# Kernel optimization log

Measured on AMD Instinct MI355X. Metric: run time of the kernel, lower is better.

Reference implementation:

```python
import jax, jax.numpy as jnp
import numpy as np

N_USERS = 100_000
N_ENTITIES = 400_000
N_NODES = N_USERS + N_ENTITIES  # 500k
DIM = 64
N_EDGES = 2_000_000
BATCH = 4096
N_LAYERS = 3
CF_WEIGHT = 1.0
L2_REG = 1e-4


def setup_inputs() -> dict:
    key = jax.random.key(0)
    k_emb, k_e, k_u, k_p, k_n = jax.random.split(key, 5)
    # xavier_uniform on (N, D): bound = sqrt(6/(N+D))
    bound = float(np.sqrt(6.0 / (N_NODES + DIM)))
    emb = jax.random.uniform(k_emb, (N_NODES, DIM), jnp.float32, -bound, bound)
    edge_index = jax.random.randint(k_e, (2, N_EDGES), 0, N_NODES, dtype=jnp.int32)
    user_idx = jax.random.randint(k_u, (BATCH,), 0, N_USERS, dtype=jnp.int32)
    pos_item = jax.random.randint(k_p, (BATCH,), 0, N_NODES, dtype=jnp.int32)
    neg_item = jax.random.randint(k_n, (BATCH,), 0, N_NODES, dtype=jnp.int32)
    return {"emb": emb, "edge_index": edge_index, "user_idx": user_idx,
            "pos_item": pos_item, "neg_item": neg_item}


def _lightgcn(emb, edge_index, n_layers):
    # LGConv(normalize=True): x' = D^{-1/2} A D^{-1/2} x, no self loops.
    n = emb.shape[0]
    src, dst = edge_index[0], edge_index[1]
    deg = jax.ops.segment_sum(jnp.ones_like(dst, dtype=emb.dtype), dst,
                              num_segments=n)
    dinv = jnp.where(deg > 0, jax.lax.rsqrt(jnp.maximum(deg, 1e-12)), 0.0)
    norm = dinv[src] * dinv[dst]  # [E]
    x = emb
    acc = emb  # layer-0 term of the mean over stacked layers
    for _ in range(n_layers):
        msgs = x[src] * norm[:, None]  # [E, D] gather + scale
        x = jax.ops.segment_sum(msgs, dst, num_segments=n)  # scatter-add
        acc = acc + x
    return acc / (n_layers + 1)  # mean over (layers+1) stacked embeddings


def reference(emb, edge_index, user_idx, pos_item, neg_item):
    all_layer = _lightgcn(emb, edge_index, N_LAYERS)
    u = all_layer[user_idx]
    p = all_layer[pos_item]
    n_ = all_layer[neg_item]
    pos_score = jnp.sum(u * p, axis=-1)
    neg_score = jnp.sum(u * n_, axis=-1)
    # BPRLoss: -mean(logsigmoid(pos - neg)) == mean(softplus(neg - pos))
    cf_loss = jnp.mean(jax.nn.softplus(neg_score - pos_score))
    u_ego = emb[user_idx]
    p_ego = emb[pos_item]
    n_ego = emb[neg_item]
    reg_loss = 0.5 * (jnp.sum(u_ego ** 2) + jnp.sum(p_ego ** 2)
                      + jnp.sum(n_ego ** 2)) / float(BATCH)
    return CF_WEIGHT * cf_loss + L2_REG * reg_loss
```

## Files before the change

kernel.cpp:

```cpp
#include <hip/hip_runtime.h>
#include <cstdint>
#include <cstddef>

#define N_USERS   100000
#define N_NODES   500000
#define DIM       64
#define N_EDGES   2000000
#define BATCH     4096
#define SCAN_B    1024
#define NBLK      ((N_NODES + SCAN_B - 1) / SCAN_B)
#define X1C_CAP   350000
#define LA_CAP    150000

__global__ void k_deg(const int* __restrict__ dst, int* __restrict__ deg) {
    int t = blockIdx.x * blockDim.x + threadIdx.x;
    if (t < N_EDGES / 4) {
        int4 d = ((const int4*)dst)[t];
        atomicAdd(&deg[d.x], 1); atomicAdd(&deg[d.y], 1);
        atomicAdd(&deg[d.z], 1); atomicAdd(&deg[d.w], 1);
    }
}

__global__ void k_scan1(const int* __restrict__ v, int* __restrict__ bsum) {
    __shared__ int s[SCAN_B];
    int i = blockIdx.x * SCAN_B + threadIdx.x;
    s[threadIdx.x] = (i < N_NODES) ? v[i] : 0;
    __syncthreads();
    for (int off = SCAN_B / 2; off; off >>= 1) {
        if (threadIdx.x < off) s[threadIdx.x] += s[threadIdx.x + off];
        __syncthreads();
    }
    if (threadIdx.x == 0) bsum[blockIdx.x] = s[0];
}

__global__ void k_scan2(const int* __restrict__ bsum, int* __restrict__ boff,
                        int* __restrict__ tail, int tail_val) {
    __shared__ int s[512];
    int v = (threadIdx.x < NBLK) ? bsum[threadIdx.x] : 0;
    s[threadIdx.x] = v;
    __syncthreads();
    for (int off = 1; off < 512; off <<= 1) {
        int t = (threadIdx.x >= off) ? s[threadIdx.x - off] : 0;
        __syncthreads();
        s[threadIdx.x] += t;
        __syncthreads();
    }
    if (threadIdx.x < NBLK) boff[threadIdx.x] = s[threadIdx.x] - v;
    if (threadIdx.x == 0 && tail) tail[0] = tail_val;
}

__global__ void k_scan3(const int* __restrict__ deg, const int* __restrict__ boff,
                        int* __restrict__ rowstart, int* __restrict__ cursor,
                        float* __restrict__ dinv) {
    __shared__ int s[SCAN_B];
    int i = blockIdx.x * SCAN_B + threadIdx.x;
    int v = (i < N_NODES) ? deg[i] : 0;
    s[threadIdx.x] = v;
    __syncthreads();
    for (int off = 1; off < SCAN_B; off <<= 1) {
        int t = (threadIdx.x >= off) ? s[threadIdx.x - off] : 0;
        __syncthreads();
        s[threadIdx.x] += t;
        __syncthreads();
    }
    if (i < N_NODES) {
        int ex = s[threadIdx.x] - v + boff[blockIdx.x];
        rowstart[i] = ex;
        cursor[i] = ex;
        dinv[i] = (v > 0) ? rsqrtf((float)v) : 0.0f;
    }
}

__global__ void k_scan1f(const unsigned char* __restrict__ fA,
                         const unsigned char* __restrict__ fB,
                         int* __restrict__ bsumP) {
    __shared__ int s[SCAN_B];
    int i = blockIdx.x * SCAN_B + threadIdx.x;
    int v = 0;
    if (i < N_NODES) v = (int)fA[i] | ((int)fB[i] << 16);
    s[threadIdx.x] = v;
    __syncthreads();
    for (int off = SCAN_B / 2; off; off >>= 1) {
        if (threadIdx.x < off) s[threadIdx.x] += s[threadIdx.x + off];
        __syncthreads();
    }
    if (threadIdx.x == 0) bsumP[blockIdx.x] = s[0];
}

__global__ void k_scan2f(const int* __restrict__ bsumP, int* __restrict__ boffA,
                         int* __restrict__ boffB, int* __restrict__ counts) {
    __shared__ int sA[512];
    __shared__ int sB[512];
    int p = (threadIdx.x < NBLK) ? bsumP[threadIdx.x] : 0;
    int vA = p & 0xFFFF, vB = p >> 16;
    sA[threadIdx.x] = vA; sB[threadIdx.x] = vB;
    __syncthreads();
    for (int off = 1; off < 512; off <<= 1) {
        int tA = (threadIdx.x >= off) ? sA[threadIdx.x - off] : 0;
        int tB = (threadIdx.x >= off) ? sB[threadIdx.x - off] : 0;
        __syncthreads();
        sA[threadIdx.x] += tA; sB[threadIdx.x] += tB;
        __syncthreads();
    }
    if (threadIdx.x < NBLK) {
        boffA[threadIdx.x] = sA[threadIdx.x] - vA;
        boffB[threadIdx.x] = sB[threadIdx.x] - vB;
    }
    if (threadIdx.x == 511) { counts[0] = sA[511]; counts[1] = sB[511]; }
}

__global__ void k_scan3f(const unsigned char* __restrict__ fA,
                         const unsigned char* __restrict__ fB,
                         const int* __restrict__ boffA, const int* __restrict__ boffB,
                         int* __restrict__ mapB, int* __restrict__ listA,
                         int* __restrict__ listB) {
    __shared__ int s[SCAN_B];
    int i = blockIdx.x * SCAN_B + threadIdx.x;
    int a = 0, b = 0;
    if (i < N_NODES) { a = (int)fA[i]; b = (int)fB[i]; }
    int v = a | (b << 16);
    s[threadIdx.x] = v;
    __syncthreads();
    for (int off = 1; off < SCAN_B; off <<= 1) {
        int t = (threadIdx.x >= off) ? s[threadIdx.x - off] : 0;
        __syncthreads();
        s[threadIdx.x] += t;
        __syncthreads();
    }
    if (i < N_NODES) {
        int inc = s[threadIdx.x];
        int exA = (inc & 0xFFFF) - a + boffA[blockIdx.x];
        int exB = (inc >> 16) - b + boffB[blockIdx.x];
        if (a) listA[exA] = i;
        mapB[i] = b ? exB : -1;
        if (b) listB[exB] = i;
    }
}

__global__ void k_scatter(const int* __restrict__ src, const int* __restrict__ dst,
                          const unsigned char* __restrict__ fB,
                          int* __restrict__ cursor, int* __restrict__ csr_src) {
    int t = blockIdx.x * blockDim.x + threadIdx.x;
    if (t < N_EDGES / 4) {
        int4 s = ((const int4*)src)[t];
        int4 d = ((const int4*)dst)[t];
        if (fB[d.x]) csr_src[atomicAdd(&cursor[d.x], 1)] = s.x;
        if (fB[d.y]) csr_src[atomicAdd(&cursor[d.y], 1)] = s.y;
        if (fB[d.z]) csr_src[atomicAdd(&cursor[d.z], 1)] = s.z;
        if (fB[d.w]) csr_src[atomicAdd(&cursor[d.w], 1)] = s.w;
    }
}

__global__ void k_mark(const int* __restrict__ u, const int* __restrict__ p,
                       const int* __restrict__ n, unsigned char* __restrict__ f3,
                       unsigned char* __restrict__ fA, unsigned char* __restrict__ fB) {
    int i = blockIdx.x * blockDim.x + threadIdx.x;
    if (i >= 3 * BATCH) return;
    int idx;
    if (i < BATCH)          idx = u[i];
    else if (i < 2 * BATCH) idx = p[i - BATCH];
    else                    idx = n[i - 2 * BATCH];
    f3[idx] = 1; fA[idx] = 1; fB[idx] = 1;
}

__global__ void k_expand_edges(const int* __restrict__ src, const int* __restrict__ dst,
                               const unsigned char* __restrict__ fin,
                               unsigned char* __restrict__ fout) {
    int t = blockIdx.x * blockDim.x + threadIdx.x;
    if (t < N_EDGES / 4) {
        int4 s = ((const int4*)src)[t];
        int4 d = ((const int4*)dst)[t];
        if (fin[d.x] && !fout[s.x]) fout[s.x] = 1;
        if (fin[d.y] && !fout[s.y]) fout[s.y] = 1;
        if (fin[d.z] && !fout[s.z]) fout[s.z] = 1;
        if (fin[d.w] && !fout[s.w]) fout[s.w] = 1;
    }
}

__global__ void k_prop1(const float* __restrict__ emb, const int* __restrict__ listB,
                        const int* __restrict__ counts,
                        const float* __restrict__ dinv, const int* __restrict__ rowstart,
                        const int* __restrict__ csr_src, float* __restrict__ x1c) {
    int lane = threadIdx.x & 63;
    int wv = (blockIdx.x * blockDim.x + threadIdx.x) >> 6;
    if (wv >= counts[1]) return;
    int node = listB[wv];
    int sub = lane >> 4, q = lane & 15;
    int b = rowstart[node], e = rowstart[node + 1];
    float4 acc = {0.f, 0.f, 0.f, 0.f};
    for (int i = b + sub; i < e; i += 4) {
        int s = csr_src[i];
        float dv = dinv[s];
        float4 v = ((const float4*)(emb + (size_t)s * DIM))[q];
        acc.x += v.x * dv; acc.y += v.y * dv; acc.z += v.z * dv; acc.w += v.w * dv;
    }
    for (int off = 16; off <= 32; off <<= 1) {
        acc.x += __shfl_xor(acc.x, off, 64);
        acc.y += __shfl_xor(acc.y, off, 64);
        acc.z += __shfl_xor(acc.z, off, 64);
        acc.w += __shfl_xor(acc.w, off, 64);
    }
    if (sub == 0) {
        float dw = dinv[node];
        float4 o = {acc.x * dw, acc.y * dw, acc.z * dw, acc.w * dw};
        ((float4*)x1c)[(size_t)wv * 16 + q] = o;
    }
}

__global__ void k_prop2(const float* __restrict__ x1c, const int* __restrict__ mapB,
                        const int* __restrict__ listA, const int* __restrict__ counts,
                        const float* __restrict__ dinv, const int* __restrict__ rowstart,
                        const int* __restrict__ csr_src, float* __restrict__ x2) {
    int lane = threadIdx.x & 63;
    int wv = (blockIdx.x * blockDim.x + threadIdx.x) >> 6;
    if (wv >= counts[0]) return;
    int node = listA[wv];
    int sub = lane >> 4, q = lane & 15;
    int b = rowstart[node], e = rowstart[node + 1];
    float4 acc = {0.f, 0.f, 0.f, 0.f};
    for (int i = b + sub; i < e; i += 4) {
        int s = csr_src[i];
        float dv = dinv[s];
        float4 v = ((const float4*)(x1c + (size_t)mapB[s] * DIM))[q];
        acc.x += v.x * dv; acc.y += v.y * dv; acc.z += v.z * dv; acc.w += v.w * dv;
    }
    for (int off = 16; off <= 32; off <<= 1) {
        acc.x += __shfl_xor(acc.x, off, 64);
        acc.y += __shfl_xor(acc.y, off, 64);
        acc.z += __shfl_xor(acc.z, off, 64);
        acc.w += __shfl_xor(acc.w, off, 64);
    }
    if (sub == 0) {
        float dw = dinv[node];
        float4 o = {acc.x * dw, acc.y * dw, acc.z * dw, acc.w * dw};
        ((float4*)(x2 + (size_t)node * DIM))[q] = o;
    }
}

__global__ void k_prop3(const float* __restrict__ x2,
                        const int* __restrict__ u, const int* __restrict__ p,
                        const int* __restrict__ n,
                        const float* __restrict__ dinv, const int* __restrict__ rowstart,
                        const int* __restrict__ csr_src, float* __restrict__ x3c) {
    int lane = threadIdx.x & 63;
    int wv = (blockIdx.x * blockDim.x + threadIdx.x) >> 6;
    if (wv >= 3 * BATCH) return;
    int t;
    if (wv < BATCH)          t = u[wv];
    else if (wv < 2 * BATCH) t = p[wv - BATCH];
    else                     t = n[wv - 2 * BATCH];
    int sub = lane >> 4, q = lane & 15;
    int b = rowstart[t], e = rowstart[t + 1];
    float4 acc = {0.f, 0.f, 0.f, 0.f};
    for (int i = b + sub; i < e; i += 4) {
        int s = csr_src[i];
        float dv = dinv[s];
        float4 v = ((const float4*)(x2 + (size_t)s * DIM))[q];
        acc.x += v.x * dv; acc.y += v.y * dv; acc.z += v.z * dv; acc.w += v.w * dv;
    }
    for (int off = 16; off <= 32; off <<= 1) {
        acc.x += __shfl_xor(acc.x, off, 64);
        acc.y += __shfl_xor(acc.y, off, 64);
        acc.z += __shfl_xor(acc.z, off, 64);
        acc.w += __shfl_xor(acc.w, off, 64);
    }
    if (sub == 0) {
        float dw = dinv[t];
        float4 o = {acc.x * dw, acc.y * dw, acc.z * dw, acc.w * dw};
        ((float4*)x3c)[(size_t)wv * 16 + q] = o;
    }
}

__global__ void k_loss(const float* __restrict__ emb, const float* __restrict__ x1c,
                       const float* __restrict__ x2, const float* __restrict__ x3c,
                       const int* __restrict__ mapB,
                       const int* __restrict__ u, const int* __restrict__ p,
                       const int* __restrict__ n, float* __restrict__ out) {
    int lane = threadIdx.x & 63;
    int w = (blockIdx.x * blockDim.x + threadIdx.x) >> 6;
    if (w >= BATCH) return;
    int ui = u[w], pi = p[w], ni = n[w];
    float ue = emb[(size_t)ui * DIM + lane];
    float pe = emb[(size_t)pi * DIM + lane];
    float ne = emb[(size_t)ni * DIM + lane];
    float uall = 0.25f * (ue + x1c[(size_t)mapB[ui] * DIM + lane]
                             + x2[(size_t)ui * DIM + lane]
                             + x3c[(size_t)w * DIM + lane]);
    float pall = 0.25f * (pe + x1c[(size_t)mapB[pi] * DIM + lane]
                             + x2[(size_t)pi * DIM + lane]
                             + x3c[(size_t)(BATCH + w) * DIM + lane]);
    float nall = 0.25f * (ne + x1c[(size_t)mapB[ni] * DIM + lane]
                             + x2[(size_t)ni * DIM + lane]
                             + x3c[(size_t)(2 * BATCH + w) * DIM + lane]);
    float pos = uall * pall;
    float neg = uall * nall;
    float sq  = ue * ue + pe * pe + ne * ne;
    for (int off = 32; off; off >>= 1) {
        pos += __shfl_xor(pos, off, 64);
        neg += __shfl_xor(neg, off, 64);
        sq  += __shfl_xor(sq,  off, 64);
    }
    if (lane == 0) {
        float z = neg - pos;
        float sp = fmaxf(z, 0.0f) + log1pf(expf(-fabsf(z)));
        float contrib = sp * (1.0f / BATCH) + 1e-4f * 0.5f * sq * (1.0f / BATCH);
        atomicAdd(out, contrib);
    }
}

extern "C" void kernel_launch(void* const* d_in, const int* in_sizes, int n_in,
                              void* d_out, int out_size, void* d_ws, size_t ws_size,
                              hipStream_t stream) {
    const float* emb  = (const float*)d_in[0];
    const int*   edge = (const int*)d_in[1];
    const int*   src  = edge;
    const int*   dst  = edge + N_EDGES;
    const int*   uidx = (const int*)d_in[2];
    const int*   pidx = (const int*)d_in[3];
    const int*   nidx = (const int*)d_in[4];
    float* out = (float*)d_out;

    char* w = (char*)d_ws;
    float* x2       = (float*)w;                 w += (size_t)N_NODES * DIM * 4;
    float* x1c      = (float*)w;                 w += (size_t)X1C_CAP * DIM * 4;
    float* x3c      = (float*)w;                 w += (size_t)3 * BATCH * DIM * 4;
    float* dinv     = (float*)w;                 w += (size_t)N_NODES * 4;
    int*   deg      = (int*)w;                   w += (size_t)N_NODES * 4;
    int*   rowstart = (int*)w;                   w += (size_t)(N_NODES + 4) * 4;
    int*   cursor   = (int*)w;                   w += (size_t)N_NODES * 4;
    int*   csr_src  = (int*)w;                   w += (size_t)N_EDGES * 4;
    int*   mapB     = (int*)w;                   w += (size_t)N_NODES * 4;
    int*   listB    = (int*)w;                   w += (size_t)X1C_CAP * 4;
    int*   listA    = (int*)w;                   w += (size_t)LA_CAP * 4;
    unsigned char* flags = (unsigned char*)w;    w += (size_t)3 * N_NODES;
    unsigned char* f3 = flags;
    unsigned char* fA = flags + N_NODES;
    unsigned char* fB = flags + 2 * N_NODES;
    int*   bsum     = (int*)w;                   w += (size_t)NBLK * 4;
    int*   boff     = (int*)w;                   w += (size_t)NBLK * 4;
    int*   bsumP    = (int*)w;                   w += (size_t)NBLK * 4;
    int*   boffA    = (int*)w;                   w += (size_t)NBLK * 4;
    int*   boffB    = (int*)w;                   w += (size_t)NBLK * 4;
    int*   counts   = (int*)w;                   w += 16;

    hipMemsetAsync(deg, 0, (size_t)N_NODES * 4, stream);
    hipMemsetAsync(flags, 0, (size_t)3 * N_NODES, stream);
    hipMemsetAsync(out, 0, 4, stream);

    k_mark<<<(3 * BATCH + 255) / 256, 256, 0, stream>>>(uidx, pidx, nidx, f3, fA, fB);
    k_expand_edges<<<(N_EDGES / 4 + 255) / 256, 256, 0, stream>>>(src, dst, f3, fA);
    k_expand_edges<<<(N_EDGES / 4 + 255) / 256, 256, 0, stream>>>(src, dst, fA, fB);

    k_deg<<<(N_EDGES / 4 + 255) / 256, 256, 0, stream>>>(dst, deg);
    k_scan1<<<NBLK, SCAN_B, 0, stream>>>(deg, bsum);
    k_scan2<<<1, 512, 0, stream>>>(bsum, boff, rowstart + N_NODES, N_EDGES);
    k_scan3<<<NBLK, SCAN_B, 0, stream>>>(deg, boff, rowstart, cursor, dinv);
    k_scatter<<<(N_EDGES / 4 + 255) / 256, 256, 0, stream>>>(src, dst, fB, cursor, csr_src);

    k_scan1f<<<NBLK, SCAN_B, 0, stream>>>(fA, fB, bsumP);
    k_scan2f<<<1, 512, 0, stream>>>(bsumP, boffA, boffB, counts);
    k_scan3f<<<NBLK, SCAN_B, 0, stream>>>(fA, fB, boffA, boffB, mapB, listA, listB);

    const int PT = 256;
    k_prop1<<<((size_t)X1C_CAP * 64 + PT - 1) / PT, PT, 0, stream>>>(
        emb, listB, counts, dinv, rowstart, csr_src, x1c);
    k_prop2<<<((size_t)LA_CAP * 64 + PT - 1) / PT, PT, 0, stream>>>(
        x1c, mapB, listA, counts, dinv, rowstart, csr_src, x2);
    k_prop3<<<(3 * BATCH * 64 + PT - 1) / PT, PT, 0, stream>>>(
        x2, uidx, pidx, nidx, dinv, rowstart, csr_src, x3c);

    k_loss<<<(BATCH * 64 + 255) / 256, 256, 0, stream>>>(
        emb, x1c, x2, x3c, mapB, uidx, pidx, nidx, out);
}
```

Baseline: 529.5 us.

## Store propagated embeddings as pre-scaled bf16 and fuse degree, expansion and scan passes

Embeddings are pre-multiplied by dinv and stored as bf16. Intermediate layers are likewise stored as bf16 scaled by dinv squared, so gathers move half the bytes and skip the per-edge dinv lookup. The degree count is fused into the first frontier expansion, and the two three-kernel scans are merged into one shared scan. That scan emits per-node int4 records holding row range and dinv. Layer 2 output is compacted instead of using a full N×64 buffer, at the cost of bf16 rounding error in the loss and an extra full-table conversion pass.

Measured after the change: 501.9 us. 1.05x faster.

```diff
diff --git a/kernel.cpp b/kernel.cpp
--- a/kernel.cpp
+++ b/kernel.cpp
@@ -12,133 +12,165 @@
 #define X1C_CAP   350000
 #define LA_CAP    150000
 
-__global__ void k_deg(const int* __restrict__ dst, int* __restrict__ deg) {
+typedef unsigned char uchar;
+typedef unsigned short ushort;
+typedef unsigned int uint;
+
+__device__ __forceinline__ ushort f2bf(float f) {
+    uint u = __float_as_uint(f);
+    uint r = u + 0x7FFFu + ((u >> 16) & 1u);
+    return (ushort)(r >> 16);
+}
+__device__ __forceinline__ float bflo(uint u) { return __uint_as_float(u << 16); }
+__device__ __forceinline__ float bfhi(uint u) { return __uint_as_float(u & 0xFFFF0000u); }
+
+__global__ void k_degexp(const int* __restrict__ src, const int* __restrict__ dst,
+                         int* __restrict__ deg, const uchar* __restrict__ f3,
+                         uchar* __restrict__ fA) {
     int t = blockIdx.x * blockDim.x + threadIdx.x;
     if (t < N_EDGES / 4) {
+        int4 s = ((const int4*)src)[t];
         int4 d = ((const int4*)dst)[t];
         atomicAdd(&deg[d.x], 1); atomicAdd(&deg[d.y], 1);
         atomicAdd(&deg[d.z], 1); atomicAdd(&deg[d.w], 1);
-    }
-}
-
-__global__ void k_scan1(const int* __restrict__ v, int* __restrict__ bsum) {
-    __shared__ int s[SCAN_B];
+        if (f3[d.x] && !fA[s.x]) fA[s.x] = 1;
+        if (f3[d.y] && !fA[s.y]) fA[s.y] = 1;
+        if (f3[d.z] && !fA[s.z]) fA[s.z] = 1;
+        if (f3[d.w] && !fA[s.w]) fA[s.w] = 1;
+    }
+}
+
+__global__ void k_expand(const int* __restrict__ src, const int* __restrict__ dst,
+                         const uchar* __restrict__ fin, uchar* __restrict__ fout) {
+    int t = blockIdx.x * blockDim.x + threadIdx.x;
+    if (t < N_EDGES / 4) {
+        int4 s = ((const int4*)src)[t];
+        int4 d = ((const int4*)dst)[t];
+        if (fin[d.x] && !fout[s.x]) fout[s.x] = 1;
+        if (fin[d.y] && !fout[s.y]) fout[s.y] = 1;
+        if (fin[d.z] && !fout[s.z]) fout[s.z] = 1;
+        if (fin[d.w] && !fout[s.w]) fout[s.w] = 1;
+    }
+}
+
+__global__ void k_mark(const int* __restrict__ u, const int* __restrict__ p,
+                       const int* __restrict__ n, uchar* __restrict__ f3,
+                       uchar* __restrict__ fA, uchar* __restrict__ fB) {
+    int i = blockIdx.x * blockDim.x + threadIdx.x;
+    if (i >= 3 * BATCH) return;
+    int idx;
+    if (i < BATCH)          idx = u[i];
+    else if (i < 2 * BATCH) idx = p[i - BATCH];
+    else                    idx = n[i - 2 * BATCH];
+    f3[idx] = 1; fA[idx] = 1; fB[idx] = 1;
+}
+
+__global__ void k_scanA(const int* __restrict__ deg, const uchar* __restrict__ fA,
+                        const uchar* __restrict__ fB, int* __restrict__ bsumD,
+                        int* __restrict__ bsumP) {
+    __shared__ int sD[SCAN_B];
+    __shared__ int sP[SCAN_B];
     int i = blockIdx.x * SCAN_B + threadIdx.x;
-    s[threadIdx.x] = (i < N_NODES) ? v[i] : 0;
+    int d = 0, pk = 0;
+    if (i < N_NODES) { d = deg[i]; pk = (int)fA[i] | ((int)fB[i] << 16); }
+    sD[threadIdx.x] = d; sP[threadIdx.x] = pk;
     __syncthreads();
     for (int off = SCAN_B / 2; off; off >>= 1) {
-        if (threadIdx.x < off) s[threadIdx.x] += s[threadIdx.x + off];
-        __syncthreads();
-    }
-    if (threadIdx.x == 0) bsum[blockIdx.x] = s[0];
-}
-
-__global__ void k_scan2(const int* __restrict__ bsum, int* __restrict__ boff,
-                        int* __restrict__ tail, int tail_val) {
-    __shared__ int s[512];
-    int v = (threadIdx.x < NBLK) ? bsum[threadIdx.x] : 0;
-    s[threadIdx.x] = v;
+        if (threadIdx.x < off) {
+            sD[threadIdx.x] += sD[threadIdx.x + off];
+            sP[threadIdx.x] += sP[threadIdx.x + off];
+        }
+        __syncthreads();
+    }
+    if (threadIdx.x == 0) { bsumD[blockIdx.x] = sD[0]; bsumP[blockIdx.x] = sP[0]; }
+}
+
+__global__ void k_scanB(const int* __restrict__ bsumD, const int* __restrict__ bsumP,
+                        int* __restrict__ boffD, int* __restrict__ boffA,
+                        int* __restrict__ boffB, int* __restrict__ counts,
+                        int* __restrict__ rowstart_tail) {
+    __shared__ int sD[512];
+    __shared__ int sA[512];
+    __shared__ int sB[512];
+    int d = (threadIdx.x < NBLK) ? bsumD[threadIdx.x] : 0;
+    int p = (threadIdx.x < NBLK) ? bsumP[threadIdx.x] : 0;
+    int a = p & 0xFFFF, b = p >> 16;
+    sD[threadIdx.x] = d; sA[threadIdx.x] = a; sB[threadIdx.x] = b;
     __syncthreads();
     for (int off = 1; off < 512; off <<= 1) {
-        int t = (threadIdx.x >= off) ? s[threadIdx.x - off] : 0;
-        __syncthreads();
-        s[threadIdx.x] += t;
-        __syncthreads();
-    }
-    if (threadIdx.x < NBLK) boff[threadIdx.x] = s[threadIdx.x] - v;
-    if (threadIdx.x == 0 && tail) tail[0] = tail_val;
-}
-
-__global__ void k_scan3(const int* __restrict__ deg, const int* __restrict__ boff,
+        int tD = (threadIdx.x >= off) ? sD[threadIdx.x - off] : 0;
+        int tA = (threadIdx.x >= off) ? sA[threadIdx.x - off] : 0;
+        int tB = (threadIdx.x >= off) ? sB[threadIdx.x - off] : 0;
+        __syncthreads();
+        sD[threadIdx.x] += tD; sA[threadIdx.x] += tA; sB[threadIdx.x] += tB;
+        __syncthreads();
+    }
+    if (threadIdx.x < NBLK) {
+        boffD[threadIdx.x] = sD[threadIdx.x] - d;
+        boffA[threadIdx.x] = sA[threadIdx.x] - a;
+        boffB[threadIdx.x] = sB[threadIdx.x] - b;
+    }
+    if (threadIdx.x == 511) {
+        counts[0] = sA[511]; counts[1] = sB[511];
+        rowstart_tail[0] = N_EDGES;
+    }
+}
+
+__global__ void k_scanC(const int* __restrict__ deg, const uchar* __restrict__ fA,
+                        const uchar* __restrict__ fB,
+                        const int* __restrict__ boffD, const int* __restrict__ boffA,
+                        const int* __restrict__ boffB,
                         int* __restrict__ rowstart, int* __restrict__ cursor,
-                        float* __restrict__ dinv) {
-    __shared__ int s[SCAN_B];
+                        float* __restrict__ dinv, int* __restrict__ mapA,
+                        int* __restrict__ mapB, int4* __restrict__ listA4,
+                        int4* __restrict__ listB4) {
+    __shared__ int sD[SCAN_B];
+    __shared__ int sP[SCAN_B];
     int i = blockIdx.x * SCAN_B + threadIdx.x;
-    int v = (i < N_NODES) ? deg[i] : 0;
-    s[threadIdx.x] = v;
+    int d = 0, a = 0, b = 0;
+    if (i < N_NODES) { d = deg[i]; a = (int)fA[i]; b = (int)fB[i]; }
+    sD[threadIdx.x] = d; sP[threadIdx.x] = a | (b << 16);
     __syncthreads();
     for (int off = 1; off < SCAN_B; off <<= 1) {
-        int t = (threadIdx.x >= off) ? s[threadIdx.x - off] : 0;
-        __syncthreads();
-        s[threadIdx.x] += t;
+        int tD = (threadIdx.x >= off) ? sD[threadIdx.x - off] : 0;
+        int tP = (threadIdx.x >= off) ? sP[threadIdx.x - off] : 0;
+        __syncthreads();
+        sD[threadIdx.x] += tD; sP[threadIdx.x] += tP;
         __syncthreads();
     }
     if (i < N_NODES) {
-        int ex = s[threadIdx.x] - v + boff[blockIdx.x];
-        rowstart[i] = ex;
-        cursor[i] = ex;
-        dinv[i] = (v > 0) ? rsqrtf((float)v) : 0.0f;
-    }
-}
-
-__global__ void k_scan1f(const unsigned char* __restrict__ fA,
-                         const unsigned char* __restrict__ fB,
-                         int* __restrict__ bsumP) {
-    __shared__ int s[SCAN_B];
-    int i = blockIdx.x * SCAN_B + threadIdx.x;
-    int v = 0;
-    if (i < N_NODES) v = (int)fA[i] | ((int)fB[i] << 16);
-    s[threadIdx.x] = v;
-    __syncthreads();
-    for (int off = SCAN_B / 2; off; off >>= 1) {
-        if (threadIdx.x < off) s[threadIdx.x] += s[threadIdx.x + off];
-        __syncthreads();
-    }
-    if (threadIdx.x == 0) bsumP[blockIdx.x] = s[0];
-}
-
-__global__ void k_scan2f(const int* __restrict__ bsumP, int* __restrict__ boffA,
-                         int* __restrict__ boffB, int* __restrict__ counts) {
-    __shared__ int sA[512];
-    __shared__ int sB[512];
-    int p = (threadIdx.x < NBLK) ? bsumP[threadIdx.x] : 0;
-    int vA = p & 0xFFFF, vB = p >> 16;
-    sA[threadIdx.x] = vA; sB[threadIdx.x] = vB;
-    __syncthreads();
-    for (int off = 1; off < 512; off <<= 1) {
-        int tA = (threadIdx.x >= off) ? sA[threadIdx.x - off] : 0;
-        int tB = (threadIdx.x >= off) ? sB[threadIdx.x - off] : 0;
-        __syncthreads();
-        sA[threadIdx.x] += tA; sB[threadIdx.x] += tB;
-        __syncthreads();
-    }
-    if (threadIdx.x < NBLK) {
-        boffA[threadIdx.x] = sA[threadIdx.x] - vA;
-        boffB[threadIdx.x] = sB[threadIdx.x] - vB;
-    }
-    if (threadIdx.x == 511) { counts[0] = sA[511]; counts[1] = sB[511]; }
-}
-
-__global__ void k_scan3f(const unsigned char* __restrict__ fA,
-                         const unsigned char* __restrict__ fB,
-                         const int* __restrict__ boffA, const int* __restrict__ boffB,
-                         int* __restrict__ mapB, int* __restrict__ listA,
-                         int* __restrict__ listB) {
-    __shared__ int s[SCAN_B];
-    int i = blockIdx.x * SCAN_B + threadIdx.x;
-    int a = 0, b = 0;
-    if (i < N_NODES) { a = (int)fA[i]; b = (int)fB[i]; }
-    int v = a | (b << 16);
-    s[threadIdx.x] = v;
-    __syncthreads();
-    for (int off = 1; off < SCAN_B; off <<= 1) {
-        int t = (threadIdx.x >= off) ? s[threadIdx.x - off] : 0;
-        __syncthreads();
-        s[threadIdx.x] += t;
-        __syncthreads();
-    }
-    if (i < N_NODES) {
-        int inc = s[threadIdx.x];
-        int exA = (inc & 0xFFFF) - a + boffA[blockIdx.x];
-        int exB = (inc >> 16) - b + boffB[blockIdx.x];
-        if (a) listA[exA] = i;
+        int exD = sD[threadIdx.x] - d + boffD[blockIdx.x];
+        int incP = sP[threadIdx.x];
+        int exA = (incP & 0xFFFF) - a + boffA[blockIdx.x];
+        int exB = (incP >> 16) - b + boffB[blockIdx.x];
+        rowstart[i] = exD;
+        cursor[i] = exD;
+        float dv = (d > 0) ? rsqrtf((float)d) : 0.0f;
+        dinv[i] = dv;
+        mapA[i] = a ? exA : -1;
         mapB[i] = b ? exB : -1;
-        if (b) listB[exB] = i;
+        int4 ent = make_int4(exD, exD + d, __float_as_int(dv), 0);
+        if (a) listA4[exA] = ent;
+        if (b) listB4[exB] = ent;
+    }
+}
+
+__global__ void k_conv(const float* __restrict__ emb, const float* __restrict__ dinv,
+                       ushort* __restrict__ embs) {
+    int c = blockIdx.x * blockDim.x + threadIdx.x;
+    if (c < N_NODES * 16) {
+        int row = c >> 4;
+        float4 v = ((const float4*)emb)[c];
+        float dv = dinv[row];
+        uint2 o;
+        o.x = (uint)f2bf(v.x * dv) | ((uint)f2bf(v.y * dv) << 16);
+        o.y = (uint)f2bf(v.z * dv) | ((uint)f2bf(v.w * dv) << 16);
+        ((uint2*)embs)[c] = o;
     }
 }
 
 __global__ void k_scatter(const int* __restrict__ src, const int* __restrict__ dst,
-                          const unsigned char* __restrict__ fB,
+                          const uchar* __restrict__ fB,
                           int* __restrict__ cursor, int* __restrict__ csr_src) {
     int t = blockIdx.x * blockDim.x + threadIdx.x;
     if (t < N_EDGES / 4) {
@@ -151,48 +183,20 @@
     }
 }
 
-__global__ void k_mark(const int* __restrict__ u, const int* __restrict__ p,
-                       const int* __restrict__ n, unsigned char* __restrict__ f3,
-                       unsigned char* __restrict__ fA, unsigned char* __restrict__ fB) {
-    int i = blockIdx.x * blockDim.x + threadIdx.x;
-    if (i >= 3 * BATCH) return;
-    int idx;
-    if (i < BATCH)          idx = u[i];
-    else if (i < 2 * BATCH) idx = p[i - BATCH];
-    else                    idx = n[i - 2 * BATCH];
-    f3[idx] = 1; fA[idx] = 1; fB[idx] = 1;
-}
-
-__global__ void k_expand_edges(const int* __restrict__ src, const int* __restrict__ dst,
-                               const unsigned char* __restrict__ fin,
-                               unsigned char* __restrict__ fout) {
-    int t = blockIdx.x * blockDim.x + threadIdx.x;
-    if (t < N_EDGES / 4) {
-        int4 s = ((const int4*)src)[t];
-        int4 d = ((const int4*)dst)[t];
-        if (fin[d.x] && !fout[s.x]) fout[s.x] = 1;
-        if (fin[d.y] && !fout[s.y]) fout[s.y] = 1;
-        if (fin[d.z] && !fout[s.z]) fout[s.z] = 1;
-        if (fin[d.w] && !fout[s.w]) fout[s.w] = 1;
-    }
-}
-
-__global__ void k_prop1(const float* __restrict__ emb, const int* __restrict__ listB,
-                        const int* __restrict__ counts,
-                        const float* __restrict__ dinv, const int* __restrict__ rowstart,
-                        const int* __restrict__ csr_src, float* __restrict__ x1c) {
+__global__ void k_prop1(const ushort* __restrict__ embs, const int4* __restrict__ listB4,
+                        const int* __restrict__ counts, const int* __restrict__ csr_src,
+                        ushort* __restrict__ x1c) {
     int lane = threadIdx.x & 63;
     int wv = (blockIdx.x * blockDim.x + threadIdx.x) >> 6;
     if (wv >= counts[1]) return;
-    int node = listB[wv];
+    int4 nb = listB4[wv];
     int sub = lane >> 4, q = lane & 15;
-    int b = rowstart[node], e = rowstart[node + 1];
     float4 acc = {0.f, 0.f, 0.f, 0.f};
-    for (int i = b + sub; i < e; i += 4) {
+    for (int i = nb.x + sub; i < nb.y; i += 4) {
         int s = csr_src[i];
-        float dv = dinv[s];
-        float4 v = ((const float4*)(emb + (size_t)s * DIM))[q];
-        acc.x += v.x * dv; acc.y += v.y * dv; acc.z += v.z * dv; acc.w += v.w * dv;
+        uint2 u = *(const uint2*)(embs + (size_t)s * DIM + q * 4);
+        acc.x += bflo(u.x); acc.y += bfhi(u.x);
+        acc.z += bflo(u.y); acc.w += bfhi(u.y);
     }
     for (int off = 16; off <= 32; off <<= 1) {
         acc.x += __shfl_xor(acc.x, off, 64);
@@ -201,28 +205,30 @@
         acc.w += __shfl_xor(acc.w, off, 64);
     }
     if (sub == 0) {
-        float dw = dinv[node];
-        float4 o = {acc.x * dw, acc.y * dw, acc.z * dw, acc.w * dw};
-        ((float4*)x1c)[(size_t)wv * 16 + q] = o;
-    }
-}
-
-__global__ void k_prop2(const float* __restrict__ x1c, const int* __restrict__ mapB,
-                        const int* __restrict__ listA, const int* __restrict__ counts,
-                        const float* __restrict__ dinv, const int* __restrict__ rowstart,
-                        const int* __restrict__ csr_src, float* __restrict__ x2) {
+        float dv = __int_as_float(nb.z);
+        float d2 = dv * dv;
+        uint2 o;
+        o.x = (uint)f2bf(acc.x * d2) | ((uint)f2bf(acc.y * d2) << 16);
+        o.y = (uint)f2bf(acc.z * d2) | ((uint)f2bf(acc.w * d2) << 16);
+        *(uint2*)(x1c + (size_t)wv * DIM + q * 4) = o;
+    }
+}
+
+__global__ void k_prop2(const ushort* __restrict__ x1c, const int* __restrict__ mapB,
+                        const int4* __restrict__ listA4, const int* __restrict__ counts,
+                        const int* __restrict__ csr_src, ushort* __restrict__ x2c) {
     int lane = threadIdx.x & 63;
     int wv = (blockIdx.x * blockDim.x + threadIdx.x) >> 6;
     if (wv >= counts[0]) return;
-    int node = listA[wv];
+    int4 nb = listA4[wv];
     int sub = lane >> 4, q = lane & 15;
-    int b = rowstart[node], e = rowstart[node + 1];
     float4 acc = {0.f, 0.f, 0.f, 0.f};
-    for (int i = b + sub; i < e; i += 4) {
+    for (int i = nb.x + sub; i < nb.y; i += 4) {
         int s = csr_src[i];
-        float dv = dinv[s];
-        float4 v = ((const float4*)(x1c + (size_t)mapB[s] * DIM))[q];
-        acc.x += v.x * dv; acc.y += v.y * dv; acc.z += v.z * dv; acc.w += v.w * dv;
+        int slot = mapB[s];
+        uint2 u = *(const uint2*)(x1c + (size_t)slot * DIM + q * 4);
+        acc.x += bflo(u.x); acc.y += bfhi(u.x);
+        acc.z += bflo(u.y); acc.w += bfhi(u.y);
     }
     for (int off = 16; off <= 32; off <<= 1) {
         acc.x += __shfl_xor(acc.x, off, 64);
@@ -231,17 +237,20 @@
         acc.w += __shfl_xor(acc.w, off, 64);
     }
     if (sub == 0) {
-        float dw = dinv[node];
-        float4 o = {acc.x * dw, acc.y * dw, acc.z * dw, acc.w * dw};
-        ((float4*)(x2 + (size_t)node * DIM))[q] = o;
-    }
-}
-
-__global__ void k_prop3(const float* __restrict__ x2,
+        float dv = __int_as_float(nb.z);
+        float d2 = dv * dv;
+        uint2 o;
+        o.x = (uint)f2bf(acc.x * d2) | ((uint)f2bf(acc.y * d2) << 16);
+        o.y = (uint)f2bf(acc.z * d2) | ((uint)f2bf(acc.w * d2) << 16);
+        *(uint2*)(x2c + (size_t)wv * DIM + q * 4) = o;
+    }
+}
+
+__global__ void k_prop3(const ushort* __restrict__ x2c, const int* __restrict__ mapA,
                         const int* __restrict__ u, const int* __restrict__ p,
-                        const int* __restrict__ n,
-                        const float* __restrict__ dinv, const int* __restrict__ rowstart,
-                        const int* __restrict__ csr_src, float* __restrict__ x3c) {
+                        const int* __restrict__ n, const float* __restrict__ dinv,
+                        const int* __restrict__ rowstart, const int* __restrict__ csr_src,
+                        float* __restrict__ x3c) {
     int lane = threadIdx.x & 63;
     int wv = (blockIdx.x * blockDim.x + threadIdx.x) >> 6;
     if (wv >= 3 * BATCH) return;
@@ -254,9 +263,10 @@
     float4 acc = {0.f, 0.f, 0.f, 0.f};
     for (int i = b + sub; i < e; i += 4) {
         int s = csr_src[i];
-        float dv = dinv[s];
-        float4 v = ((const float4*)(x2 + (size_t)s * DIM))[q];
-        acc.x += v.x * dv; acc.y += v.y * dv; acc.z += v.z * dv; acc.w += v.w * dv;
+        int slot = mapA[s];
+        uint2 uu = *(const uint2*)(x2c + (size_t)slot * DIM + q * 4);
+        acc.x += bflo(uu.x); acc.y += bfhi(uu.x);
+        acc.z += bflo(uu.y); acc.w += bfhi(uu.y);
     }
     for (int off = 16; off <= 32; off <<= 1) {
         acc.x += __shfl_xor(acc.x, off, 64);
@@ -265,33 +275,38 @@
         acc.w += __shfl_xor(acc.w, off, 64);
     }
     if (sub == 0) {
-        float dw = dinv[t];
-        float4 o = {acc.x * dw, acc.y * dw, acc.z * dw, acc.w * dw};
+        float dv = dinv[t];
+        float4 o = {acc.x * dv, acc.y * dv, acc.z * dv, acc.w * dv};
         ((float4*)x3c)[(size_t)wv * 16 + q] = o;
     }
 }
 
-__global__ void k_loss(const float* __restrict__ emb, const float* __restrict__ x1c,
-                       const float* __restrict__ x2, const float* __restrict__ x3c,
-                       const int* __restrict__ mapB,
+__global__ void k_loss(const float* __restrict__ emb, const ushort* __restrict__ x1c,
+                       const ushort* __restrict__ x2c, const float* __restrict__ x3c,
+                       const int* __restrict__ mapA, const int* __restrict__ mapB,
+                       const float* __restrict__ dinv,
                        const int* __restrict__ u, const int* __restrict__ p,
                        const int* __restrict__ n, float* __restrict__ out) {
     int lane = threadIdx.x & 63;
     int w = (blockIdx.x * blockDim.x + threadIdx.x) >> 6;
     if (w >= BATCH) return;
     int ui = u[w], pi = p[w], ni = n[w];
+    float dvu = dinv[ui], dvp = dinv[pi], dvn = dinv[ni];
+    float rdu = dvu > 0.f ? 1.f / dvu : 0.f;
+    float rdp = dvp > 0.f ? 1.f / dvp : 0.f;
+    float rdn = dvn > 0.f ? 1.f / dvn : 0.f;
     float ue = emb[(size_t)ui * DIM + lane];
     float pe = emb[(size_t)pi * DIM + lane];
     float ne = emb[(size_t)ni * DIM + lane];
-    float uall = 0.25f * (ue + x1c[(size_t)mapB[ui] * DIM + lane]
-                             + x2[(size_t)ui * DIM + lane]
-                             + x3c[(size_t)w * DIM + lane]);
-    float pall = 0.25f * (pe + x1c[(size_t)mapB[pi] * DIM + lane]
-                             + x2[(size_t)pi * DIM + lane]
-                             + x3c[(size_t)(BATCH + w) * DIM + lane]);
-    float nall = 0.25f * (ne + x1c[(size_t)mapB[ni] * DIM + lane]
-                             + x2[(size_t)ni * DIM + lane]
-                             + x3c[(size_t)(2 * BATCH + w) * DIM + lane]);
+    float u1 = __uint_as_float((uint)x1c[(size_t)mapB[ui] * DIM + lane] << 16) * rdu;
+    float p1 = __uint_as_float((uint)x1c[(size_t)mapB[pi] * DIM + lane] << 16) * rdp;
+    float n1 = __uint_as_float((uint)x1c[(size_t)mapB[ni] * DIM + lane] << 16) * rdn;
+    float u2 = __uint_as_float((uint)x2c[(size_t)mapA[ui] * DIM + lane] << 16) * rdu;
+    float p2 = __uint_as_float((uint)x2c[(size_t)mapA[pi] * DIM + lane] << 16) * rdp;
+    float n2 = __uint_as_float((uint)x2c[(size_t)mapA[ni] * DIM + lane] << 16) * rdn;
+    float uall = 0.25f * (ue + u1 + u2 + x3c[(size_t)w * DIM + lane]);
+    float pall = 0.25f * (pe + p1 + p2 + x3c[(size_t)(BATCH + w) * DIM + lane]);
+    float nall = 0.25f * (ne + n1 + n2 + x3c[(size_t)(2 * BATCH + w) * DIM + lane]);
     float pos = uall * pall;
     float neg = uall * nall;
     float sq  = ue * ue + pe * pe + ne * ne;
@@ -321,54 +336,57 @@
     float* out = (float*)d_out;
 
     char* w = (char*)d_ws;
-    float* x2       = (float*)w;                 w += (size_t)N_NODES * DIM * 4;
-    float* x1c      = (float*)w;                 w += (size_t)X1C_CAP * DIM * 4;
-    float* x3c      = (float*)w;                 w += (size_t)3 * BATCH * DIM * 4;
-    float* dinv     = (float*)w;                 w += (size_t)N_NODES * 4;
-    int*   deg      = (int*)w;                   w += (size_t)N_NODES * 4;
-    int*   rowstart = (int*)w;                   w += (size_t)(N_NODES + 4) * 4;
-    int*   cursor   = (int*)w;                   w += (size_t)N_NODES * 4;
-    int*   csr_src  = (int*)w;                   w += (size_t)N_EDGES * 4;
-    int*   mapB     = (int*)w;                   w += (size_t)N_NODES * 4;
-    int*   listB    = (int*)w;                   w += (size_t)X1C_CAP * 4;
-    int*   listA    = (int*)w;                   w += (size_t)LA_CAP * 4;
-    unsigned char* flags = (unsigned char*)w;    w += (size_t)3 * N_NODES;
-    unsigned char* f3 = flags;
-    unsigned char* fA = flags + N_NODES;
-    unsigned char* fB = flags + 2 * N_NODES;
-    int*   bsum     = (int*)w;                   w += (size_t)NBLK * 4;
-    int*   boff     = (int*)w;                   w += (size_t)NBLK * 4;
-    int*   bsumP    = (int*)w;                   w += (size_t)NBLK * 4;
-    int*   boffA    = (int*)w;                   w += (size_t)NBLK * 4;
-    int*   boffB    = (int*)w;                   w += (size_t)NBLK * 4;
-    int*   counts   = (int*)w;                   w += 16;
+    ushort* embs    = (ushort*)w;                w += (size_t)N_NODES * DIM * 2;
+    ushort* x1c     = (ushort*)w;                w += (size_t)X1C_CAP * DIM * 2;
+    ushort* x2c     = (ushort*)w;                w += (size_t)LA_CAP * DIM * 2;
+    float*  x3c     = (float*)w;                 w += (size_t)3 * BATCH * DIM * 4;
+    float*  dinv    = (float*)w;                 w += (size_t)N_NODES * 4;
+    int*    deg     = (int*)w;                   w += (size_t)N_NODES * 4;
+    int*    rowstart= (int*)w;                   w += (size_t)(N_NODES + 4) * 4;
+    int*    cursor  = (int*)w;                   w += (size_t)N_NODES * 4;
+    int*    csr_src = (int*)w;                   w += (size_t)N_EDGES * 4;
+    int*    mapA    = (int*)w;                   w += (size_t)N_NODES * 4;
+    int*    mapB    = (int*)w;                   w += (size_t)N_NODES * 4;
+    int4*   listA4  = (int4*)w;                  w += (size_t)LA_CAP * 16;
+    int4*   listB4  = (int4*)w;                  w += (size_t)X1C_CAP * 16;
+    uchar*  flags   = (uchar*)w;                 w += (size_t)3 * N_NODES;
+    uchar*  f3 = flags;
+    uchar*  fA = flags + N_NODES;
+    uchar*  fB = flags + 2 * N_NODES;
+    int*    bsumD   = (int*)w;                   w += (size_t)NBLK * 4;
+    int*    boffD   = (int*)w;                   w += (size_t)NBLK * 4;
+    int*    bsumP   = (int*)w;                   w += (size_t)NBLK * 4;
+    int*    boffA   = (int*)w;                   w += (size_t)NBLK * 4;
+    int*    boffB   = (int*)w;                   w += (size_t)NBLK * 4;
+    int*    counts  = (int*)w;                   w += 16;
 
     hipMemsetAsync(deg, 0, (size_t)N_NODES * 4, stream);
     hipMemsetAsync(flags, 0, (size_t)3 * N_NODES, stream);
     hipMemsetAsync(out, 0, 4, stream);
 
     k_mark<<<(3 * BATCH + 255) / 256, 256, 0, stream>>>(uidx, pidx, nidx, f3, fA, fB);
-    k_expand_edges<<<(N_EDGES / 4 + 255) / 256, 256, 0, stream>>>(src, dst, f3, fA);
-    k_expand_edges<<<(N_EDGES / 4 + 255) / 256, 256, 0, stream>>>(src, dst, fA, fB);
-
-    k_deg<<<(N_EDGES / 4 + 255) / 256, 256, 0, stream>>>(dst, deg);
-    k_scan1<<<NBLK, SCAN_B, 0, stream>>>(deg, bsum);
-    k_scan2<<<1, 512, 0, stream>>>(bsum, boff, rowstart + N_NODES, N_EDGES);
-    k_scan3<<<NBLK, SCAN_B, 0, stream>>>(deg, boff, rowstart, cursor, dinv);
+    k_degexp<<<(N_EDGES / 4 + 255) / 256, 256, 0, stream>>>(src, dst, deg, f3, fA);
+    k_expand<<<(N_EDGES / 4 + 255) / 256, 256, 0, stream>>>(src, dst, fA, fB);
+
+    k_scanA<<<NBLK, SCAN_B, 0, stream>>>(deg, fA, fB, bsumD, bsumP);
+    k_scanB<<<1, 512, 0, stream>>>(bsumD, bsumP, boffD, boffA, boffB, counts,
+                                   rowstart + N_NODES);
+    k_scanC<<<NBLK, SCAN_B, 0, stream>>>(deg, fA, fB, boffD, boffA, boffB,
+                                         rowstart, cursor, dinv, mapA, mapB,
+                                         listA4, listB4);
+
+    k_conv<<<(N_NODES * 16 + 255) / 256, 256, 0, stream>>>(emb, dinv, embs);
+
     k_scatter<<<(N_EDGES / 4 + 255) / 256, 256, 0, stream>>>(src, dst, fB, cursor, csr_src);
-
-    k_scan1f<<<NBLK, SCAN_B, 0, stream>>>(fA, fB, bsumP);
-    k_scan2f<<<1, 512, 0, stream>>>(bsumP, boffA, boffB, counts);
-    k_scan3f<<<NBLK, SCAN_B, 0, stream>>>(fA, fB, boffA, boffB, mapB, listA, listB);
 
     const int PT = 256;
     k_prop1<<<((size_t)X1C_CAP * 64 + PT - 1) / PT, PT, 0, stream>>>(
-        emb, listB, counts, dinv, rowstart, csr_src, x1c);
+        embs, listB4, counts, csr_src, x1c);
     k_prop2<<<((size_t)LA_CAP * 64 + PT - 1) / PT, PT, 0, stream>>>(
-        x1c, mapB, listA, counts, dinv, rowstart, csr_src, x2);
+        x1c, mapB, listA4, counts, csr_src, x2c);
     k_prop3<<<(3 * BATCH * 64 + PT - 1) / PT, PT, 0, stream>>>(
-        x2, uidx, pidx, nidx, dinv, rowstart, csr_src, x3c);
+        x2c, mapA, uidx, pidx, nidx, dinv, rowstart, csr_src, x3c);
 
     k_loss<<<(BATCH * 64 + 255) / 256, 256, 0, stream>>>(
-        emb, x1c, x2, x3c, mapB, uidx, pidx, nidx, out);
-}
+        emb, x1c, x2c, x3c, mapA, mapB, dinv, uidx, pidx, nidx, out);
+}
```
